# Kernel optimization log

Measured on AMD Instinct MI355X. Metric: run time of the kernel, lower is better.

The kernel has to match this reference:

```python
import math
import jax, jax.numpy as jnp
import numpy as np

NUM_HEADS = 32
NUM_KV_HEADS = 8
HEAD_DIM = 128
ROPE_THETA = 10000.0


def rotate_half(x):
    x1, x2 = jnp.split(x, 2, axis=-1)
    return jnp.concatenate((-x2, x1), axis=-1)


def rope_cos_sin(seq_len, dim, dtype):
    pos = jnp.arange(seq_len, dtype=jnp.float32)[:, None]            # [S,1]
    freqs = jnp.exp(-jnp.arange(0, dim, 2, dtype=jnp.float32) * (math.log(ROPE_THETA) / dim))
    ang = pos * freqs                                                # [S,D/2]
    cos = jnp.concatenate([jnp.cos(ang), jnp.cos(ang)], axis=-1)     # [S,D]
    sin = jnp.concatenate([jnp.sin(ang), jnp.sin(ang)], axis=-1)
    # broadcast over heads: [S,1,D]
    return cos[:, None, :].astype(dtype), sin[:, None, :].astype(dtype)


def setup_inputs() -> dict:
    key = jax.random.key(0)
    k1, k2, k3, k4, k5 = jax.random.split(key, 5)
    B, S, Hd = 1, 2048, 4096
    kv_dim = NUM_KV_HEADS * HEAD_DIM
    s = 0.02
    return {
        "hidden_states": jax.random.normal(k1, (B, S, Hd), jnp.float32),
        "Wq": jax.random.normal(k2, (Hd, Hd), jnp.float32) * s,
        "Wk": jax.random.normal(k3, (kv_dim, Hd), jnp.float32) * s,
        "Wv": jax.random.normal(k4, (kv_dim, Hd), jnp.float32) * s,
        "Wo": jax.random.normal(k5, (Hd, Hd), jnp.float32) * s,
    }


def reference(hidden_states, Wq, Wk, Wv, Wo):
    B, S, _ = hidden_states.shape
    H, KV, D = NUM_HEADS, NUM_KV_HEADS, HEAD_DIM
    groups = H // KV

    q = jnp.einsum('bsh,oh->bso', hidden_states, Wq).reshape(B, S, H, D)
    k = jnp.einsum('bsh,oh->bso', hidden_states, Wk).reshape(B, S, KV, D)
    v = jnp.einsum('bsh,oh->bso', hidden_states, Wv).reshape(B, S, KV, D)

    # GQA: repeat_interleave along head dim
    k = jnp.repeat(k, groups, axis=2)   # [B,S,H,D]
    v = jnp.repeat(v, groups, axis=2)

    cos, sin = rope_cos_sin(S, D, hidden_states.dtype)  # [S,1,D]
    q = q * cos + rotate_half(q) * sin
    k = k * cos + rotate_half(k) * sin

    q = q.transpose(0, 2, 1, 3)  # [B,H,S,D]
    k = k.transpose(0, 2, 1, 3)
    v = v.transpose(0, 2, 1, 3)

    scores = jnp.einsum('bhqd,bhkd->bhqk', q, k) / math.sqrt(D)
    causal = jnp.tril(jnp.ones((S, S), dtype=bool))
    scores = jnp.where(causal, scores, jnp.asarray(-1e9, scores.dtype))
    attn = jax.nn.softmax(scores, axis=-1)

    out = jnp.einsum('bhqk,bhkd->bqhd', attn, v).reshape(B, S, H * D)
    return jnp.einsum('bso,ho->bsh', out, Wo)
```

## Files before the change

kernel.cpp:

```cpp
#include <hip/hip_runtime.h>

#define S_LEN 2048
#define HD    4096
#define NH    32
#define NKV   8
#define DH    128
#define NQKV  6144
#define QKV_STRIDE_B (NQKV * 2)

typedef __bf16 bf16_t;
typedef __bf16 bf16x8 __attribute__((ext_vector_type(8)));
typedef float  f32x4  __attribute__((ext_vector_type(4)));
typedef unsigned short ushort8v __attribute__((ext_vector_type(8)));

__device__ inline unsigned short f2bf_bits(float f) {
  unsigned int u = __builtin_bit_cast(unsigned int, f);
  unsigned int r = (u + 0x7FFFu + ((u >> 16) & 1u)) >> 16;
  return (unsigned short)r;
}
__device__ inline bf16_t f2bf(float f) {
  return __builtin_bit_cast(bf16_t, f2bf_bits(f));
}
__device__ inline float bf2f(bf16_t b) {
  unsigned int u = ((unsigned int)__builtin_bit_cast(unsigned short, b)) << 16;
  return __builtin_bit_cast(float, u);
}

__device__ inline void load_lds16(const void* g, void* l) {
  __builtin_amdgcn_global_load_lds(
      (__attribute__((address_space(1))) unsigned int*)(void*)g,
      (__attribute__((address_space(3))) unsigned int*)l, 16, 0, 0);
}

__device__ inline void store_out(float* p, float v)  { *p = v; }
__device__ inline void store_out(bf16_t* p, float v) { *p = f2bf(v); }

__global__ void cvt_kernel(const float* __restrict__ in, bf16_t* __restrict__ out, int n8) {
  int stride = gridDim.x * blockDim.x;
  for (int i = blockIdx.x * blockDim.x + threadIdx.x; i < n8; i += stride) {
    float4 v0 = reinterpret_cast<const float4*>(in)[i * 2];
    float4 v1 = reinterpret_cast<const float4*>(in)[i * 2 + 1];
    ushort8v o;
    o[0] = f2bf_bits(v0.x); o[1] = f2bf_bits(v0.y);
    o[2] = f2bf_bits(v0.z); o[3] = f2bf_bits(v0.w);
    o[4] = f2bf_bits(v1.x); o[5] = f2bf_bits(v1.y);
    o[6] = f2bf_bits(v1.z); o[7] = f2bf_bits(v1.w);
    reinterpret_cast<ushort8v*>(out)[i] = o;
  }
}

template <typename OutT>
__global__ __launch_bounds__(256)
void gemm_bt_kernel(const bf16_t* __restrict__ A, const bf16_t* __restrict__ B,
                    OutT* __restrict__ C, int M, int N, int K, int nbx) {
  __shared__ __align__(16) bf16_t lA[128 * 32];
  __shared__ __align__(16) bf16_t lB[128 * 32];
  const int t = threadIdx.x;
  const int lane = t & 63, wave = t >> 6;

  const int nwg = gridDim.x;
  const int orig = blockIdx.x;
  const int xcd = orig & 7;
  const int qq = nwg >> 3, rr = nwg & 7;
  const int base = (xcd < rr) ? xcd * (qq + 1) : rr * (qq + 1) + (xcd - rr) * qq;
  const int wgid = base + (orig >> 3);
  const int row0 = (wgid / nbx) * 128, col0 = (wgid % nbx) * 128;

  const int wm = (wave >> 1) * 64, wn = (wave & 1) * 64;

  const int rA = wave * 32 + (lane >> 2);
  const int cA = (lane & 3) * 8;
  const char* Asrc0 = (const char*)(A + (size_t)(row0 + rA) * K + cA);
  const char* Asrc1 = (const char*)(A + (size_t)(row0 + rA + 16) * K + cA);
  const char* Bsrc0 = (const char*)(B + (size_t)(col0 + rA) * K + cA);
  const char* Bsrc1 = (const char*)(B + (size_t)(col0 + rA + 16) * K + cA);
  char* lAd = (char*)lA + wave * 2048;
  char* lBd = (char*)lB + wave * 2048;

  f32x4 acc[4][4] = {};
  const int fr = lane & 15, fq = lane >> 4;

  for (int k0 = 0; k0 < K; k0 += 32) {
    const size_t kb = (size_t)k0 * 2;
    load_lds16(Asrc0 + kb, lAd);
    load_lds16(Asrc1 + kb, lAd + 1024);
    load_lds16(Bsrc0 + kb, lBd);
    load_lds16(Bsrc1 + kb, lBd + 1024);
    __syncthreads();
    bf16x8 af[4], bfv[4];
#pragma unroll
    for (int mi = 0; mi < 4; mi++)
      af[mi] = *reinterpret_cast<const bf16x8*>(&lA[(wm + mi * 16 + fr) * 32 + fq * 8]);
#pragma unroll
    for (int ni = 0; ni < 4; ni++)
      bfv[ni] = *reinterpret_cast<const bf16x8*>(&lB[(wn + ni * 16 + fr) * 32 + fq * 8]);
#pragma unroll
    for (int mi = 0; mi < 4; mi++)
#pragma unroll
      for (int ni = 0; ni < 4; ni++)
        acc[mi][ni] = __builtin_amdgcn_mfma_f32_16x16x32_bf16(af[mi], bfv[ni], acc[mi][ni], 0, 0, 0);
    __syncthreads();
  }

#pragma unroll
  for (int mi = 0; mi < 4; mi++) {
#pragma unroll
    for (int r = 0; r < 4; r++) {
      int row = row0 + wm + mi * 16 + fq * 4 + r;
      OutT* Cp = C + (size_t)row * N + col0 + wn + fr;
#pragma unroll
      for (int ni = 0; ni < 4; ni++) store_out(Cp + ni * 16, acc[mi][ni][r]);
    }
  }
}

__global__ void rope_kernel(bf16_t* __restrict__ x, int heads, int rstride, float scale) {
  int idx = blockIdx.x * blockDim.x + threadIdx.x;
  int i = idx & 63;
  int h = (idx >> 6) % heads;
  int s = idx / (64 * heads);
  const float NEG_LOG1E4_64 = -0.14391156f;
  float freq = __expf((float)i * NEG_LOG1E4_64);
  float ang = (float)s * freq;
  float sn, cs;
  __sincosf(ang, &sn, &cs);
  bf16_t* p = x + (size_t)s * rstride + h * DH;
  float x1 = bf2f(p[i]);
  float x2 = bf2f(p[i + 64]);
  p[i]      = f2bf((x1 * cs - x2 * sn) * scale);
  p[i + 64] = f2bf((x2 * cs + x1 * sn) * scale);
}

__global__ void transpose_kernel(const bf16_t* __restrict__ in, bf16_t* __restrict__ out,
                                 int R, int C, int in_rstride) {
  __shared__ bf16_t tile[64][65];
  int c0 = blockIdx.x * 64, r0 = blockIdx.y * 64;
  int t = threadIdx.x;
#pragma unroll
  for (int i = 0; i < 16; i++) {
    int idx = t + i * 256;
    int r = idx >> 6, c = idx & 63;
    tile[r][c] = in[(size_t)(r0 + r) * in_rstride + c0 + c];
  }
  __syncthreads();
#pragma unroll
  for (int i = 0; i < 16; i++) {
    int idx = t + i * 256;
    int r = idx >> 6, c = idx & 63;
    out[(size_t)(c0 + r) * R + r0 + c] = tile[c][r];
  }
}

__global__ __launch_bounds__(256)
void attn_kernel(const bf16_t* __restrict__ Qkv, const bf16_t* __restrict__ Vt,
                 bf16_t* __restrict__ O) {
  __shared__ __align__(16) char lK[2][64 * 256];
  __shared__ __align__(16) char lV[2][64 * 256];
  __shared__ __align__(16) bf16_t lP[4][16 * 72];

  const int t = threadIdx.x, lane = t & 63, wave = t >> 6;
  const int h = blockIdx.y, kvh = h >> 2;
  const int pid = blockIdx.x;
  const int fr = lane & 15, fq = lane >> 4;

  const int gc = wave * 4 + (lane >> 4);
  const int sS = (lane & 15) ^ (gc & 15);
  const char* KsrcB = (const char*)(Qkv + HD + (size_t)kvh * DH) +
                      (size_t)gc * QKV_STRIDE_B + sS * 16;
  const int dVc = gc * 2 + (sS >> 3);
  const char* VsrcB = (const char*)Vt + (size_t)kvh * DH * S_LEN * 2 +
                      (size_t)dVc * 4096 + (sS & 7) * 16;
  char* dKw = (char*)lK[0] + wave * 1024;
  char* dVw = (char*)lV[0] + wave * 1024;

  auto stage = [&](int buf, int kv0) {
    char* dk = dKw + buf * (64 * 256);
    char* dv = dVw + buf * (64 * 256);
    const char* ks = KsrcB + (size_t)kv0 * QKV_STRIDE_B;
    const char* vs = VsrcB + (size_t)kv0 * 2;
#pragma unroll
    for (int i = 0; i < 4; i++) {
      load_lds16(ks + i * (16 * QKV_STRIDE_B), dk + i * 4096);
      load_lds16(vs + i * (size_t)(32 * 4096), dv + i * 4096);
    }
  };

  stage(0, 0);
  int buf = 0;

  for (int pass = 0; pass < 2; pass++) {
    const int qb = pass ? pid : (31 - pid);
    const int q0 = qb * 64 + wave * 16;

    bf16x8 qf[4];
    const bf16_t* Qp = Qkv + (size_t)(q0 + fr) * NQKV + h * DH + fq * 8;
#pragma unroll
    for (int kt = 0; kt < 4; kt++)
      qf[kt] = *reinterpret_cast<const bf16x8*>(Qp + kt * 32);

    f32x4 o_acc[8] = {};
    float m_run[4] = {-1e30f, -1e30f, -1e30f, -1e30f};
    float l_run[4] = {0.f, 0.f, 0.f, 0.f};

    for (int tt = 0; tt <= qb; tt++) {
      __syncthreads();
      if (tt < qb)            stage(buf ^ 1, (tt + 1) * 64);
      else if (pass == 0)     stage(buf ^ 1, 0);

      const char* cK = lK[buf];
      const char* cV = lV[buf];
      const bool diag = (tt == qb);

      f32x4 s_acc[4] = {};
      __builtin_amdgcn_s_setprio(1);
#pragma unroll
      for (int nt = 0; nt < 4; nt++) {
        const char* rowp = cK + (nt * 16 + fr) * 256;
#pragma unroll
        for (int kt = 0; kt < 4; kt++) {
          const bf16x8 kf = *reinterpret_cast<const bf16x8*>(
              rowp + (((kt * 4 + fq) ^ fr) << 4));
          s_acc[nt] = __builtin_amdgcn_mfma_f32_16x16x32_bf16(qf[kt], kf, s_acc[nt], 0, 0, 0);
        }
      }
      __builtin_amdgcn_s_setprio(0);

      float pmax[4];
#pragma unroll
      for (int r = 0; r < 4; r++) {
        if (diag) {
          const int qrel = wave * 16 + fq * 4 + r;
#pragma unroll
          for (int nt = 0; nt < 4; nt++)
            if (nt * 16 + fr > qrel) s_acc[nt][r] = -1e30f;
        }
        float mr = fmaxf(fmaxf(s_acc[0][r], s_acc[1][r]), fmaxf(s_acc[2][r], s_acc[3][r]));
#pragma unroll
        for (int off = 1; off < 16; off <<= 1) mr = fmaxf(mr, __shfl_xor(mr, off, 16));
        pmax[r] = mr;
      }
      bool nb = (pmax[0] > m_run[0] + 8.f) || (pmax[1] > m_run[1] + 8.f) ||
                (pmax[2] > m_run[2] + 8.f) || (pmax[3] > m_run[3] + 8.f);
      if (__any(nb)) {
#pragma unroll
        for (int r = 0; r < 4; r++) {
          float mnew = fmaxf(m_run[r], pmax[r]);
          float alpha = __expf(m_run[r] - mnew);
#pragma unroll
          for (int ni = 0; ni < 8; ni++) o_acc[ni][r] *= alpha;
          l_run[r] *= alpha;
          m_run[r] = mnew;
        }
      }
      bf16_t* lPw = lP[wave];
#pragma unroll
      for (int r = 0; r < 4; r++) {
        float p0 = __expf(s_acc[0][r] - m_run[r]);
        float p1 = __expf(s_acc[1][r] - m_run[r]);
        float p2 = __expf(s_acc[2][r] - m_run[r]);
        float p3 = __expf(s_acc[3][r] - m_run[r]);
        float sr = (p0 + p1) + (p2 + p3);
#pragma unroll
        for (int off = 1; off < 16; off <<= 1) sr += __shfl_xor(sr, off, 16);
        l_run[r] += sr;
        const int row = fq * 4 + r;
        lPw[row * 72 + fr]      = f2bf(p0);
        lPw[row * 72 + 16 + fr] = f2bf(p1);
        lPw[row * 72 + 32 + fr] = f2bf(p2);
        lPw[row * 72 + 48 + fr] = f2bf(p3);
      }

#pragma unroll
      for (int kk = 0; kk < 2; kk++) {
        const bf16x8 pf = *reinterpret_cast<const bf16x8*>(lPw + fr * 72 + kk * 32 + fq * 8);
        __builtin_amdgcn_s_setprio(1);
#pragma unroll
        for (int ni = 0; ni < 8; ni++) {
          const int d = ni * 16 + fr;
          const int g = d >> 1;
          const int slot = ((d & 1) * 8 + kk * 4 + fq) ^ (g & 15);
          const bf16x8 vf = *reinterpret_cast<const bf16x8*>(cV + g * 256 + (slot << 4));
          o_acc[ni] = __builtin_amdgcn_mfma_f32_16x16x32_bf16(pf, vf, o_acc[ni], 0, 0, 0);
        }
        __builtin_amdgcn_s_setprio(0);
      }
      buf ^= 1;
    }

#pragma unroll
    for (int r = 0; r < 4; r++) {
      int qrow = q0 + fq * 4 + r;
      float inv = 1.0f / l_run[r];
      bf16_t* Op = O + ((size_t)qrow * NH + h) * DH + fr;
#pragma unroll
      for (int ni = 0; ni < 8; ni++) Op[ni * 16] = f2bf(o_acc[ni][r] * inv);
    }
  }
}

extern "C" void kernel_launch(void* const* d_in, const int* in_sizes, int n_in,
                              void* d_out, int out_size, void* d_ws, size_t ws_size,
                              hipStream_t stream) {
  const float* X  = (const float*)d_in[0];
  const float* Wq = (const float*)d_in[1];
  const float* Wk = (const float*)d_in[2];
  const float* Wv = (const float*)d_in[3];
  const float* Wo = (const float*)d_in[4];
  float* out = (float*)d_out;

  char* ws = (char*)d_ws;
  size_t off = 0;
  auto alloc = [&](size_t bytes) {
    char* p = ws + off;
    off += (bytes + 255) & ~(size_t)255;
    return p;
  };
  const size_t kvdim = (size_t)NKV * DH;
  bf16_t* Xb    = (bf16_t*)alloc((size_t)S_LEN * HD * 2);
  bf16_t* Wqkvb = (bf16_t*)alloc((size_t)NQKV * HD * 2);
  bf16_t* Wob   = (bf16_t*)alloc((size_t)HD * HD * 2);
  bf16_t* QKVb  = (bf16_t*)alloc((size_t)S_LEN * NQKV * 2);
  bf16_t* Vtb   = (bf16_t*)alloc((size_t)S_LEN * kvdim * 2);
  bf16_t* AOb   = (bf16_t*)alloc((size_t)S_LEN * HD * 2);
  (void)ws_size;

  auto cvt = [&](const float* in, bf16_t* o, size_t n) {
    int n8 = (int)(n / 8);
    int blocks = (n8 + 255) / 256;
    if (blocks > 2048) blocks = 2048;
    cvt_kernel<<<dim3(blocks), dim3(256), 0, stream>>>(in, o, n8);
  };
  cvt(X,  Xb,    (size_t)S_LEN * HD);
  cvt(Wq, Wqkvb, (size_t)HD * HD);
  cvt(Wk, Wqkvb + (size_t)HD * HD,   kvdim * HD);
  cvt(Wv, Wqkvb + (size_t)(HD + kvdim) * HD, kvdim * HD);
  cvt(Wo, Wob,   (size_t)HD * HD);

  {
    int nbx = NQKV / 128, nby = S_LEN / 128;
    gemm_bt_kernel<bf16_t><<<dim3(nbx * nby), dim3(256), 0, stream>>>(
        Xb, Wqkvb, QKVb, S_LEN, NQKV, HD, nbx);
  }

  rope_kernel<<<dim3(S_LEN * NH * 64 / 256), dim3(256), 0, stream>>>(
      QKVb, NH, NQKV, 0.08838834764831845f);
  rope_kernel<<<dim3(S_LEN * NKV * 64 / 256), dim3(256), 0, stream>>>(
      QKVb + HD, NKV, NQKV, 1.0f);

  transpose_kernel<<<dim3((int)kvdim / 64, S_LEN / 64), dim3(256), 0, stream>>>(
      QKVb + HD + kvdim, Vtb, S_LEN, (int)kvdim, NQKV);

  attn_kernel<<<dim3(16, NH), dim3(256), 0, stream>>>(QKVb, Vtb, AOb);

  {
    int nbx = HD / 128, nby = S_LEN / 128;
    gemm_bt_kernel<float><<<dim3(nbx * nby), dim3(256), 0, stream>>>(
        AOb, Wob, out, S_LEN, HD, HD, nbx);
  }
}
```

Before: 401.1 us.

## Double-buffer GEMM LDS tiles and merge conversion and RoPE launches

The GEMM now uses two LDS buffers and prefetches the next K-tile via global_load_lds while MFMAs run on the current one. This drops one barrier per iteration and raises wave priority around the MFMA block. The five fp32-to-bf16 conversion launches become one kernel writing into the contiguous workspace, and the two RoPE launches become one. The trade is doubled LDS use per block and a reliance on the workspace buffers being adjacent.

```diff
diff --git a/kernel.cpp b/kernel.cpp
--- a/kernel.cpp
+++ b/kernel.cpp
@@ -35,26 +35,46 @@
 __device__ inline void store_out(float* p, float v)  { *p = v; }
 __device__ inline void store_out(bf16_t* p, float v) { *p = f2bf(v); }
 
-__global__ void cvt_kernel(const float* __restrict__ in, bf16_t* __restrict__ out, int n8) {
-  int stride = gridDim.x * blockDim.x;
-  for (int i = blockIdx.x * blockDim.x + threadIdx.x; i < n8; i += stride) {
-    float4 v0 = reinterpret_cast<const float4*>(in)[i * 2];
-    float4 v1 = reinterpret_cast<const float4*>(in)[i * 2 + 1];
+__global__ void cvt_all_kernel(const float* __restrict__ s0, const float* __restrict__ s1,
+                               const float* __restrict__ s2, const float* __restrict__ s3,
+                               const float* __restrict__ s4,
+                               long n0, long n1, long n2, long n3,
+                               long total, bf16_t* __restrict__ dst) {
+  long stride = (long)gridDim.x * blockDim.x;
+  for (long i = (long)blockIdx.x * blockDim.x + threadIdx.x; i < total; i += stride) {
+    const float* src;
+    long rel = i;
+    if (rel < n0) src = s0;
+    else {
+      rel -= n0;
+      if (rel < n1) src = s1;
+      else {
+        rel -= n1;
+        if (rel < n2) src = s2;
+        else {
+          rel -= n2;
+          if (rel < n3) src = s3;
+          else { rel -= n3; src = s4; }
+        }
+      }
+    }
+    float4 v0 = reinterpret_cast<const float4*>(src)[rel * 2];
+    float4 v1 = reinterpret_cast<const float4*>(src)[rel * 2 + 1];
     ushort8v o;
     o[0] = f2bf_bits(v0.x); o[1] = f2bf_bits(v0.y);
     o[2] = f2bf_bits(v0.z); o[3] = f2bf_bits(v0.w);
     o[4] = f2bf_bits(v1.x); o[5] = f2bf_bits(v1.y);
     o[6] = f2bf_bits(v1.z); o[7] = f2bf_bits(v1.w);
-    reinterpret_cast<ushort8v*>(out)[i] = o;
+    reinterpret_cast<ushort8v*>(dst)[i] = o;
   }
 }
 
 template <typename OutT>
 __global__ __launch_bounds__(256)
-void gemm_bt_kernel(const bf16_t* __restrict__ A, const bf16_t* __restrict__ B,
-                    OutT* __restrict__ C, int M, int N, int K, int nbx) {
-  __shared__ __align__(16) bf16_t lA[128 * 32];
-  __shared__ __align__(16) bf16_t lB[128 * 32];
+void gemm_db32_kernel(const bf16_t* __restrict__ A, const bf16_t* __restrict__ B,
+                      OutT* __restrict__ C, int M, int N, int K, int nbx) {
+  __shared__ __align__(16) bf16_t lA[2][128 * 32];
+  __shared__ __align__(16) bf16_t lB[2][128 * 32];
   const int t = threadIdx.x;
   const int lane = t & 63, wave = t >> 6;
 
@@ -74,32 +94,41 @@
   const char* Asrc1 = (const char*)(A + (size_t)(row0 + rA + 16) * K + cA);
   const char* Bsrc0 = (const char*)(B + (size_t)(col0 + rA) * K + cA);
   const char* Bsrc1 = (const char*)(B + (size_t)(col0 + rA + 16) * K + cA);
-  char* lAd = (char*)lA + wave * 2048;
-  char* lBd = (char*)lB + wave * 2048;
-
+
+  const int fr = lane & 15, fq = lane >> 4;
   f32x4 acc[4][4] = {};
-  const int fr = lane & 15, fq = lane >> 4;
-
-  for (int k0 = 0; k0 < K; k0 += 32) {
+
+  auto stage = [&](int b, int k0) {
     const size_t kb = (size_t)k0 * 2;
+    char* lAd = (char*)lA[b] + wave * 2048;
+    char* lBd = (char*)lB[b] + wave * 2048;
     load_lds16(Asrc0 + kb, lAd);
     load_lds16(Asrc1 + kb, lAd + 1024);
     load_lds16(Bsrc0 + kb, lBd);
     load_lds16(Bsrc1 + kb, lBd + 1024);
+  };
+
+  stage(0, 0);
+  int b = 0;
+  for (int k0 = 0; k0 < K; k0 += 32) {
     __syncthreads();
+    if (k0 + 32 < K) stage(b ^ 1, k0 + 32);
+
     bf16x8 af[4], bfv[4];
 #pragma unroll
     for (int mi = 0; mi < 4; mi++)
-      af[mi] = *reinterpret_cast<const bf16x8*>(&lA[(wm + mi * 16 + fr) * 32 + fq * 8]);
+      af[mi] = *reinterpret_cast<const bf16x8*>(&lA[b][(wm + mi * 16 + fr) * 32 + fq * 8]);
 #pragma unroll
     for (int ni = 0; ni < 4; ni++)
-      bfv[ni] = *reinterpret_cast<const bf16x8*>(&lB[(wn + ni * 16 + fr) * 32 + fq * 8]);
+      bfv[ni] = *reinterpret_cast<const bf16x8*>(&lB[b][(wn + ni * 16 + fr) * 32 + fq * 8]);
+    __builtin_amdgcn_s_setprio(1);
 #pragma unroll
     for (int mi = 0; mi < 4; mi++)
 #pragma unroll
       for (int ni = 0; ni < 4; ni++)
         acc[mi][ni] = __builtin_amdgcn_mfma_f32_16x16x32_bf16(af[mi], bfv[ni], acc[mi][ni], 0, 0, 0);
-    __syncthreads();
+    __builtin_amdgcn_s_setprio(0);
+    b ^= 1;
   }
 
 #pragma unroll
@@ -114,17 +143,19 @@
   }
 }
 
-__global__ void rope_kernel(bf16_t* __restrict__ x, int heads, int rstride, float scale) {
+__global__ void rope_all_kernel(bf16_t* __restrict__ qkv, float qscale) {
   int idx = blockIdx.x * blockDim.x + threadIdx.x;
   int i = idx & 63;
-  int h = (idx >> 6) % heads;
-  int s = idx / (64 * heads);
+  int hh = (idx >> 6) % (NH + NKV);
+  int s = idx / (64 * (NH + NKV));
   const float NEG_LOG1E4_64 = -0.14391156f;
   float freq = __expf((float)i * NEG_LOG1E4_64);
   float ang = (float)s * freq;
   float sn, cs;
   __sincosf(ang, &sn, &cs);
-  bf16_t* p = x + (size_t)s * rstride + h * DH;
+  const int colbase = (hh < NH) ? hh * DH : HD + (hh - NH) * DH;
+  const float scale = (hh < NH) ? qscale : 1.0f;
+  bf16_t* p = qkv + (size_t)s * NQKV + colbase;
   float x1 = bf2f(p[i]);
   float x2 = bf2f(p[i + 64]);
   p[i]      = f2bf((x1 * cs - x2 * sn) * scale);
@@ -324,28 +355,25 @@
   bf16_t* AOb   = (bf16_t*)alloc((size_t)S_LEN * HD * 2);
   (void)ws_size;
 
-  auto cvt = [&](const float* in, bf16_t* o, size_t n) {
-    int n8 = (int)(n / 8);
-    int blocks = (n8 + 255) / 256;
-    if (blocks > 2048) blocks = 2048;
-    cvt_kernel<<<dim3(blocks), dim3(256), 0, stream>>>(in, o, n8);
-  };
-  cvt(X,  Xb,    (size_t)S_LEN * HD);
-  cvt(Wq, Wqkvb, (size_t)HD * HD);
-  cvt(Wk, Wqkvb + (size_t)HD * HD,   kvdim * HD);
-  cvt(Wv, Wqkvb + (size_t)(HD + kvdim) * HD, kvdim * HD);
-  cvt(Wo, Wob,   (size_t)HD * HD);
+  {
+    const long n0 = (long)S_LEN * HD / 8;
+    const long n1 = (long)HD * HD / 8;
+    const long n2 = (long)kvdim * HD / 8;
+    const long n3 = (long)kvdim * HD / 8;
+    const long n4 = (long)HD * HD / 8;
+    const long total = n0 + n1 + n2 + n3 + n4;
+    cvt_all_kernel<<<dim3(2048), dim3(256), 0, stream>>>(
+        X, Wq, Wk, Wv, Wo, n0, n1, n2, n3, total, Xb);
+  }
 
   {
     int nbx = NQKV / 128, nby = S_LEN / 128;
-    gemm_bt_kernel<bf16_t><<<dim3(nbx * nby), dim3(256), 0, stream>>>(
+    gemm_db32_kernel<bf16_t><<<dim3(nbx * nby), dim3(256), 0, stream>>>(
         Xb, Wqkvb, QKVb, S_LEN, NQKV, HD, nbx);
   }
 
-  rope_kernel<<<dim3(S_LEN * NH * 64 / 256), dim3(256), 0, stream>>>(
-      QKVb, NH, NQKV, 0.08838834764831845f);
-  rope_kernel<<<dim3(S_LEN * NKV * 64 / 256), dim3(256), 0, stream>>>(
-      QKVb + HD, NKV, NQKV, 1.0f);
+  rope_all_kernel<<<dim3(S_LEN * (NH + NKV) * 64 / 256), dim3(256), 0, stream>>>(
+      QKVb, 0.08838834764831845f);
 
   transpose_kernel<<<dim3((int)kvdim / 64, S_LEN / 64), dim3(256), 0, stream>>>(
       QKVb + HD + kvdim, Vtb, S_LEN, (int)kvdim, NQKV);
@@ -354,7 +382,7 @@
 
   {
     int nbx = HD / 128, nby = S_LEN / 128;
-    gemm_bt_kernel<float><<<dim3(nbx * nby), dim3(256), 0, stream>>>(
+    gemm_db32_kernel<float><<<dim3(nbx * nby), dim3(256), 0, stream>>>(
         AOb, Wob, out, S_LEN, HD, HD, nbx);
   }
 }
```

Result: faster. 359.7 us, median of 2 (-10.3%).
